# Performance work log

Hardware: AMD Instinct MI355X
Metric: run time of the kernel (lower is better)

## Reference

```python
import jax, jax.numpy as jnp
import numpy as np

N, IN_FEAT, LAT_FEAT, OUT_FEAT = 131072, 128, 128, 256
NUM_EXPERTS, TOP_K, OMEGA = 8, 2, 30.0


def setup_inputs() -> dict:
    key = jax.random.key(0)
    ks = jax.random.split(key, 8)
    u = lambda k_, shape, lim: jax.random.uniform(k_, shape, jnp.float32, -lim, lim)
    w_lim = np.sqrt(6.0 / IN_FEAT) / OMEGA  # SIREN init for non-first layers
    return {
        "x": jax.random.normal(ks[0], (N, IN_FEAT), jnp.float32),
        "latents": jax.random.normal(ks[1], (N, LAT_FEAT), jnp.float32),
        "gate_w": u(ks[2], (IN_FEAT, NUM_EXPERTS), 1.0 / np.sqrt(IN_FEAT)),
        "gate_b": jnp.zeros((NUM_EXPERTS,), jnp.float32),
        "W": u(ks[3], (NUM_EXPERTS, IN_FEAT, OUT_FEAT), w_lim),
        "b": u(ks[4], (NUM_EXPERTS, OUT_FEAT), 1.0 / np.sqrt(IN_FEAT)),
        "Wl": u(ks[5], (NUM_EXPERTS, LAT_FEAT, 2 * OUT_FEAT), 1.0 / np.sqrt(LAT_FEAT)),
        "bl": u(ks[6], (NUM_EXPERTS, 2 * OUT_FEAT), 1.0 / np.sqrt(LAT_FEAT)),
    }


def reference(x, latents, gate_w, gate_b, W, b, Wl, bl):
    # Gating: top-k over expert logits, softmax over the selected k logits.
    logits = x @ gate_w + gate_b                      # [N, E]
    top_vals, top_idx = jax.lax.top_k(logits, TOP_K)  # [N, k]
    top_w = jax.nn.softmax(top_vals, axis=-1)         # [N, k]
    # Dense combine weights: combine[n, e] = sum_i top_w[n, i] * (top_idx[n,i]==e).
    # Mathematically identical to the masked gather/scatter loop in torch.
    combine = jnp.sum(
        jax.nn.one_hot(top_idx, NUM_EXPERTS, dtype=x.dtype) * top_w[..., None],
        axis=1,
    )  # [N, E]
    out = jnp.zeros((x.shape[0], OUT_FEAT), x.dtype)
    for e in range(NUM_EXPERTS):  # fixed small loop over experts
        h = x @ W[e] + b[e]                    # [N, out]
        lat = latents @ Wl[e] + bl[e]          # [N, 2*out]
        scale, shift = lat[:, :OUT_FEAT], lat[:, OUT_FEAT:]
        out = out + combine[:, e:e + 1] * jnp.sin(OMEGA * h * scale + shift)
    return (out, latents)
```

## Files before the change

kernel.cpp:

```cpp
#include <hip/hip_runtime.h>

#define INF_  128
#define OUTF  256
#define LATF  128
#define OUT2  512
#define NEXP  8
#define OMEGA_ 30.0f

typedef float  f32x4  __attribute__((ext_vector_type(4)));
typedef __bf16 bf16x8 __attribute__((ext_vector_type(8)));
typedef unsigned short ushort8 __attribute__((ext_vector_type(8)));

#define PACK_THREADS (NEXP * 4 * 4 * 3 * 4 * 64)
#define EXP_STRIDE   (4 * 4 * 3 * 4 * 512)
#define PH_STRIDE    6144
#define GEMM_GRID    1056

__device__ __forceinline__ unsigned short bfbits(float f) {
    unsigned int u = __builtin_bit_cast(unsigned int, f);
    return (unsigned short)((u + 0x7FFFu + ((u >> 16) & 1u)) >> 16);
}

__device__ __forceinline__ bf16x8 cvt8(f32x4 a, f32x4 b) {
    bf16x8 r;
    r[0] = (__bf16)a.x; r[1] = (__bf16)a.y; r[2] = (__bf16)a.z; r[3] = (__bf16)a.w;
    r[4] = (__bf16)b.x; r[5] = (__bf16)b.y; r[6] = (__bf16)b.z; r[7] = (__bf16)b.w;
    return r;
}

#define GLOAD_LDS16(g, l) __builtin_amdgcn_global_load_lds( \
    (const __attribute__((address_space(1))) unsigned int*)(g), \
    (__attribute__((address_space(3))) unsigned int*)(l), 16, 0, 0)

__global__ void prep_kernel(const float* __restrict__ x,
                            const float* __restrict__ lat,
                            const float* __restrict__ gw,
                            const float* __restrict__ gb,
                            const float* __restrict__ W,
                            const float* __restrict__ Wl,
                            unsigned short* __restrict__ eidx,
                            float2* __restrict__ wpair,
                            unsigned int* __restrict__ cnt,
                            float* __restrict__ lat_out,
                            unsigned short* __restrict__ Bpk,
                            int nGate)
{
    __shared__ float sgw[INF_ * NEXP];
    __shared__ int lc[64];
    const int tid = threadIdx.x;

    if ((int)blockIdx.x >= nGate) {
        const int t = ((int)blockIdx.x - nGate) * 256 + tid;
        if (t >= PACK_THREADS) return;
        const int l   = t & 63;
        const int ks  = (t >> 6) & 3;
        const int m3  = (t >> 8) % 3;
        const int g   = (t >> 8) / 3;
        const int nf  = g & 3, nc = (g >> 2) & 3, e = g >> 4;
        const int col = nc * 64 + nf * 16 + (l & 15);
        const int kb  = ks * 32 + (l >> 4) * 8;
        ushort8 o;
#pragma unroll
        for (int j = 0; j < 8; ++j) {
            float v;
            if (m3 == 0) v = W [((size_t)e * 128 + kb + j) * 256 + col];
            else         v = Wl[((size_t)e * 128 + kb + j) * 512 + col + (m3 == 2 ? 256 : 0)];
            o[j] = bfbits(v);
        }
        *(ushort8*)(Bpk + (size_t)t * 8) = o;
        return;
    }

    ((float4*)sgw)[tid] = ((const float4*)gw)[tid];
    if (tid < 64) lc[tid] = 0;
    __syncthreads();

    const int t = blockIdx.x * 256 + tid;
    float acc[8];
#pragma unroll
    for (int e = 0; e < 8; ++e) acc[e] = gb[e];
    const float4* xr = (const float4*)(x + (size_t)t * INF_);
#pragma unroll 8
    for (int i = 0; i < 32; ++i) {
        float4 v = xr[i];
#pragma unroll
        for (int j = 0; j < 4; ++j) {
            const float xk = (&v.x)[j];
            const float4 g0 = *(const float4*)&sgw[(i * 4 + j) * 8];
            const float4 g1 = *(const float4*)&sgw[(i * 4 + j) * 8 + 4];
            acc[0] += xk * g0.x; acc[1] += xk * g0.y; acc[2] += xk * g0.z; acc[3] += xk * g0.w;
            acc[4] += xk * g1.x; acc[5] += xk * g1.y; acc[6] += xk * g1.z; acc[7] += xk * g1.w;
        }
    }
    float best = -1e30f, sec = -1e30f; int bi = 0, si = 0;
#pragma unroll
    for (int e = 0; e < 8; ++e) {
        const float v = acc[e];
        if (v > best)      { sec = best; si = bi; best = v; bi = e; }
        else if (v > sec)  { sec = v; si = e; }
    }
    const float ew  = __expf(sec - best);
    const float inv = 1.0f / (1.0f + ew);
    const float wb  = inv, wsc = ew * inv;
    int emin, emax; float wmin, wmax;
    if (bi < si) { emin = bi; wmin = wb;  emax = si; wmax = wsc; }
    else         { emin = si; wmin = wsc; emax = bi; wmax = wb;  }
    const int pid = emin * 8 + emax;
    eidx[t]  = (unsigned short)pid;
    wpair[t] = make_float2(wmin, wmax);
    atomicAdd(&lc[pid], 1);
    __syncthreads();
    if (tid < 64) { if (lc[tid]) atomicAdd(&cnt[tid], (unsigned int)lc[tid]); }

    const f32x4* lr = (const f32x4*)(lat) + (size_t)blockIdx.x * 8192;
    f32x4*       lo = (f32x4*)(lat_out)   + (size_t)blockIdx.x * 8192;
#pragma unroll
    for (int i = 0; i < 32; ++i) {
        f32x4 v = lr[tid + i * 256];
        __builtin_nontemporal_store(v, &lo[tid + i * 256]);
    }
}

__global__ void scan_kernel(unsigned int* __restrict__ c, unsigned int* __restrict__ table)
{
    const int p = threadIdx.x;
    const unsigned int n = c[p];
    unsigned int s = n;
#pragma unroll
    for (int d = 1; d < 64; d <<= 1) {
        unsigned int t = __shfl_up(s, d);
        if (p >= d) s += t;
    }
    const unsigned int excl = s - n;
    c[64 + p] = excl; c[128 + p] = excl;
    const unsigned int nt = (n + 127) >> 7;
    unsigned int ts = nt;
#pragma unroll
    for (int d = 1; d < 64; d <<= 1) {
        unsigned int t = __shfl_up(ts, d);
        if (p >= d) ts += t;
    }
    const unsigned int texcl = ts - nt;
    for (unsigned int t = 0; t < nt; ++t) table[texcl + t] = (unsigned int)p | (t << 6);
    if (p == 63) c[192] = texcl + nt;
}

__global__ void scatter_kernel(const unsigned short* __restrict__ eidx,
                               const float2* __restrict__ wpair,
                               unsigned int* __restrict__ cur,
                               unsigned int* __restrict__ perm,
                               float2* __restrict__ wps)
{
    __shared__ int lc[64];
    __shared__ unsigned int lbase[64];
    const int tid = threadIdx.x;
    if (tid < 64) lc[tid] = 0;
    __syncthreads();
    const int t = blockIdx.x * 256 + tid;
    const int pid = eidx[t];
    const float2 w = wpair[t];
    const int p = atomicAdd(&lc[pid], 1);
    __syncthreads();
    if (tid < 64) { lbase[tid] = lc[tid] ? atomicAdd(&cur[tid], (unsigned int)lc[tid]) : 0u; }
    __syncthreads();
    const unsigned int q = lbase[pid] + (unsigned int)p;
    perm[q] = (unsigned int)t;
    wps[q]  = w;
}

__launch_bounds__(256, 4)
__global__ void moe_gemm_kernel(const float* __restrict__ x,
                                const float* __restrict__ lat,
                                const unsigned short* __restrict__ Bpk,
                                const float* __restrict__ bias,
                                const float* __restrict__ biasl,
                                const unsigned int* __restrict__ c,
                                const unsigned int* __restrict__ table,
                                const unsigned int* __restrict__ perm,
                                const float2* __restrict__ wps,
                                float* __restrict__ out)
{
    __shared__ __align__(16) unsigned short sB[3][2 * PH_STRIDE];
    __shared__ __align__(16) float sbias[6 * 256];

    const unsigned int ntiles = c[192];
    const unsigned int d = blockIdx.x;
    const unsigned int bid = (d & 7) * (GEMM_GRID / 8) + (d >> 3);
    if (bid >= ntiles) return;
    const unsigned int ent = table[bid];
    const int pid  = ent & 63;
    const int tile = ent >> 6;
    const int emin = pid >> 3, emax = pid & 7;
    const unsigned int cn  = c[pid];
    const unsigned int off = c[64 + pid] + (unsigned int)tile * 128u;
    const int rows = min(128, (int)(cn - (unsigned int)tile * 128u));
    const unsigned int* permS = perm + off;
    const float2* wS = wps + off;

    const int tid  = threadIdx.x;
    const int lane = tid & 63;
    const int w    = tid >> 6;
    const int lrow = lane & 15;
    const int lgrp = lane >> 4;
    const int half = tid >> 7;
    const int wh   = (tid >> 6) & 1;
    const int t7   = tid & 127;

    const int r0 = w * 32 + lrow, r1 = r0 + 16;
    const int t0 = (int)permS[min(r0, rows - 1)];
    const int t1 = (int)permS[min(r1, rows - 1)];
    const float2 w0 = wS[min(r0, rows - 1)];
    const float2 w1 = wS[min(r1, rows - 1)];
    bf16x8 ax[2][4], al[2][4];
    {
        const float* x0 = x   + (size_t)t0 * INF_;
        const float* x1 = x   + (size_t)t1 * INF_;
        const float* l0 = lat + (size_t)t0 * LATF;
        const float* l1 = lat + (size_t)t1 * LATF;
#pragma unroll
        for (int ks = 0; ks < 4; ++ks) {
            const int kb = ks * 32 + lgrp * 8;
            ax[0][ks] = cvt8(__builtin_nontemporal_load((const f32x4*)(x0 + kb)),
                             __builtin_nontemporal_load((const f32x4*)(x0 + kb + 4)));
            ax[1][ks] = cvt8(__builtin_nontemporal_load((const f32x4*)(x1 + kb)),
                             __builtin_nontemporal_load((const f32x4*)(x1 + kb + 4)));
            al[0][ks] = cvt8(__builtin_nontemporal_load((const f32x4*)(l0 + kb)),
                             __builtin_nontemporal_load((const f32x4*)(l0 + kb + 4)));
            al[1][ks] = cvt8(__builtin_nontemporal_load((const f32x4*)(l1 + kb)),
                             __builtin_nontemporal_load((const f32x4*)(l1 + kb + 4)));
        }
    }

    const unsigned short* B0 = Bpk + (size_t)emin * EXP_STRIDE;
    const unsigned short* B1 = Bpk + (size_t)emax * EXP_STRIDE;
    const unsigned short* Bh = half ? B1 : B0;

    {
        const float* bsrc =
            (w == 0) ? bias  + emin * OUTF :
            (w == 1) ? bias  + emax * OUTF :
            (w == 2) ? biasl + emin * OUT2 :
                       biasl + emin * OUT2 + 256;
        GLOAD_LDS16(bsrc + lane * 4, &sbias[w * 256]);
        if (w < 2) {
            const float* bsrc2 = (w == 0) ? biasl + emax * OUT2
                                          : biasl + emax * OUT2 + 256;
            GLOAD_LDS16(bsrc2 + lane * 4, &sbias[(4 + w) * 256]);
        }
    }

    auto STAGE = [&](int ph, int buf) {
        const unsigned short* src = Bh + (size_t)ph * PH_STRIDE + (size_t)t7 * 8;
        unsigned short* dst = &sB[buf][half * PH_STRIDE + wh * 512];
#pragma unroll
        for (int r = 0; r < 6; ++r)
            GLOAD_LDS16(src + r * 1024, dst + r * 1024);
    };

    f32x4 acc[2][3][2];
    auto COMPUTE = [&](int ph, int buf) {
        const int cb = ph * 16 + lgrp * 4;
        const f32x4 b0h = *(const f32x4*)&sbias[0 * 256 + cb];
        const f32x4 b1h = *(const f32x4*)&sbias[1 * 256 + cb];
        const f32x4 b0s = *(const f32x4*)&sbias[2 * 256 + cb];
        const f32x4 b0f = *(const f32x4*)&sbias[3 * 256 + cb];
        const f32x4 b1s = *(const f32x4*)&sbias[4 * 256 + cb];
        const f32x4 b1f = *(const f32x4*)&sbias[5 * 256 + cb];
#pragma unroll
        for (int mf = 0; mf < 2; ++mf) {
            acc[0][0][mf] = b0h; acc[0][1][mf] = b0s; acc[0][2][mf] = b0f;
            acc[1][0][mf] = b1h; acc[1][1][mf] = b1s; acc[1][2][mf] = b1f;
        }
#pragma unroll
        for (int ex = 0; ex < 2; ++ex) {
#pragma unroll
            for (int m = 0; m < 3; ++m) {
                bf16x8 bb[4];
#pragma unroll
                for (int ks = 0; ks < 4; ++ks)
                    bb[ks] = *(const bf16x8*)&sB[buf][ex * PH_STRIDE + (m * 4 + ks) * 512 + lane * 8];
#pragma unroll
                for (int ks = 0; ks < 4; ++ks) {
#pragma unroll
                    for (int mf = 0; mf < 2; ++mf) {
                        const bf16x8 a = (m == 0) ? ax[mf][ks] : al[mf][ks];
                        acc[ex][m][mf] = __builtin_amdgcn_mfma_f32_16x16x32_bf16(bb[ks], a, acc[ex][m][mf], 0, 0, 0);
                    }
                }
            }
        }
    };

    auto EPILOGUE = [&](int ph, bool guard) {
        const int cb = ph * 16 + lgrp * 4;
#pragma unroll
        for (int mf = 0; mf < 2; ++mf) {
            const int  rr  = mf ? r1 : r0;
            if (guard && rr >= rows) continue;
            const int  tok = mf ? t1 : t0;
            const float wmn = mf ? w1.x : w0.x;
            const float wmx = mf ? w1.y : w0.y;
            const f32x4 h0 = acc[0][0][mf], s0 = acc[0][1][mf], f0 = acc[0][2][mf];
            const f32x4 h1 = acc[1][0][mf], s1 = acc[1][1][mf], f1 = acc[1][2][mf];
            f32x4 v;
#pragma unroll
            for (int j = 0; j < 4; ++j) {
                v[j] = wmn * __sinf(OMEGA_ * h0[j] * s0[j] + f0[j])
                     + wmx * __sinf(OMEGA_ * h1[j] * s1[j] + f1[j]);
            }
            __builtin_nontemporal_store(v, (f32x4*)(out + (size_t)tok * OUTF + cb));
        }
    };

    if (rows == 128) {
        STAGE(0, 0);
        STAGE(1, 1);
        asm volatile("s_waitcnt vmcnt(6)" ::: "memory");
        __builtin_amdgcn_s_barrier();
        __builtin_amdgcn_sched_barrier(0);
#pragma unroll 1
        for (int ph = 0; ph < 16; ++ph) {
            const int buf = ph % 3;
            if (ph < 14) STAGE(ph + 2, (ph + 2) % 3);
            COMPUTE(ph, buf);
            EPILOGUE(ph, false);
            __builtin_amdgcn_sched_barrier(0);
            if (ph == 0)       asm volatile("s_waitcnt vmcnt(8)" ::: "memory");
            else if (ph < 14)  asm volatile("s_waitcnt vmcnt(10)" ::: "memory");
            else if (ph == 14) asm volatile("s_waitcnt vmcnt(4)" ::: "memory");
            if (ph < 15) {
                __builtin_amdgcn_s_barrier();
                __builtin_amdgcn_sched_barrier(0);
            }
        }
    } else {
#pragma unroll 1
        for (int ph = 0; ph < 16; ++ph) {
            const int buf = ph % 3;
            STAGE(ph, buf);
            asm volatile("s_waitcnt vmcnt(0)" ::: "memory");
            __builtin_amdgcn_s_barrier();
            __builtin_amdgcn_sched_barrier(0);
            COMPUTE(ph, buf);
            EPILOGUE(ph, true);
            __builtin_amdgcn_s_barrier();
            __builtin_amdgcn_sched_barrier(0);
        }
    }
}

extern "C" void kernel_launch(void* const* d_in, const int* in_sizes, int n_in,
                              void* d_out, int out_size, void* d_ws, size_t ws_size,
                              hipStream_t stream)
{
    const float* x   = (const float*)d_in[0];
    const float* lat = (const float*)d_in[1];
    const float* gw  = (const float*)d_in[2];
    const float* gb  = (const float*)d_in[3];
    const float* W   = (const float*)d_in[4];
    const float* b   = (const float*)d_in[5];
    const float* Wl  = (const float*)d_in[6];
    const float* bl  = (const float*)d_in[7];
    float* out = (float*)d_out;
    const int N = in_sizes[0] / INF_;

    char* ws = (char*)d_ws;
    unsigned int*   cnt   = (unsigned int*)ws;
    unsigned int*   table = (unsigned int*)(ws + 1024);
    unsigned short* eidx  = (unsigned short*)(ws + 8192);
    float2*         wpair = (float2*)(ws + 8192 + 2 * (size_t)N);
    unsigned int*   perm  = (unsigned int*)(ws + 8192 + 10 * (size_t)N);
    float2*         wps   = (float2*)(ws + 8192 + 14 * (size_t)N);
    unsigned short* Bpk   = (unsigned short*)(ws + 8192 + 22 * (size_t)N);

    (void)hipMemsetAsync(cnt, 0, 256, stream);

    const int nGate = N / 256;
    prep_kernel<<<dim3(nGate + PACK_THREADS / 256), 256, 0, stream>>>(
        x, lat, gw, gb, W, Wl, eidx, wpair, cnt, out + (size_t)N * OUTF, Bpk, nGate);
    scan_kernel<<<1, 64, 0, stream>>>(cnt, table);
    scatter_kernel<<<dim3(N / 256), 256, 0, stream>>>(eidx, wpair, cnt + 128, perm, wps);

    moe_gemm_kernel<<<dim3(GEMM_GRID), 256, 0, stream>>>(x, lat, Bpk, b, bl,
                                                         cnt, table, perm, wps, out);
}
```

Baseline: 162.6 us.

## Switch B staging to double buffering, store bias as bf16, add bias in epilogue

Moves the B-weight LDS pipeline from triple to double buffering with a one-phase prefetch, cutting LDS use. Bias is converted to bf16 in shared memory and added in the epilogue instead of seeding the accumulators. Launch bounds drop to 3 waves per SIMD. This frees registers and LDS but shortens the prefetch depth and adds bf16 rounding to the bias.

```diff
diff --git a/kernel.cpp b/kernel.cpp
--- a/kernel.cpp
+++ b/kernel.cpp
@@ -25,6 +25,16 @@
     bf16x8 r;
     r[0] = (__bf16)a.x; r[1] = (__bf16)a.y; r[2] = (__bf16)a.z; r[3] = (__bf16)a.w;
     r[4] = (__bf16)b.x; r[5] = (__bf16)b.y; r[6] = (__bf16)b.z; r[7] = (__bf16)b.w;
+    return r;
+}
+
+__device__ __forceinline__ f32x4 bload(const unsigned short* p) {
+    const ushort4 u = *(const ushort4*)p;
+    f32x4 r;
+    r.x = __builtin_bit_cast(float, (unsigned int)u.x << 16);
+    r.y = __builtin_bit_cast(float, (unsigned int)u.y << 16);
+    r.z = __builtin_bit_cast(float, (unsigned int)u.z << 16);
+    r.w = __builtin_bit_cast(float, (unsigned int)u.w << 16);
     return r;
 }
 
@@ -168,7 +178,7 @@
     wps[q]  = w;
 }
 
-__launch_bounds__(256, 4)
+__launch_bounds__(256, 3)
 __global__ void moe_gemm_kernel(const float* __restrict__ x,
                                 const float* __restrict__ lat,
                                 const unsigned short* __restrict__ Bpk,
@@ -180,8 +190,8 @@
                                 const float2* __restrict__ wps,
                                 float* __restrict__ out)
 {
-    __shared__ __align__(16) unsigned short sB[3][2 * PH_STRIDE];
-    __shared__ __align__(16) float sbias[6 * 256];
+    __shared__ __align__(16) unsigned short sB[2][2 * PH_STRIDE];
+    __shared__ __align__(16) unsigned short sbias[6 * 256];
 
     const unsigned int ntiles = c[192];
     const unsigned int d = blockIdx.x;
@@ -236,16 +246,24 @@
     const unsigned short* Bh = half ? B1 : B0;
 
     {
-        const float* bsrc =
-            (w == 0) ? bias  + emin * OUTF :
-            (w == 1) ? bias  + emax * OUTF :
-            (w == 2) ? biasl + emin * OUT2 :
-                       biasl + emin * OUT2 + 256;
-        GLOAD_LDS16(bsrc + lane * 4, &sbias[w * 256]);
-        if (w < 2) {
-            const float* bsrc2 = (w == 0) ? biasl + emax * OUT2
-                                          : biasl + emax * OUT2 + 256;
-            GLOAD_LDS16(bsrc2 + lane * 4, &sbias[(4 + w) * 256]);
+        const int i4 = (tid & 63) * 4;
+        const int sg = tid >> 6;
+#pragma unroll
+        for (int rep = 0; rep < 2; ++rep) {
+            const int seg = sg + rep * 4;
+            if (seg < 6) {
+                const float* bsrc =
+                    (seg == 0) ? bias  + emin * OUTF :
+                    (seg == 1) ? bias  + emax * OUTF :
+                    (seg == 2) ? biasl + emin * OUT2 :
+                    (seg == 3) ? biasl + emin * OUT2 + 256 :
+                    (seg == 4) ? biasl + emax * OUT2 :
+                                 biasl + emax * OUT2 + 256;
+                const f32x4 v = *(const f32x4*)(bsrc + i4);
+                ushort4 u;
+                u.x = bfbits(v.x); u.y = bfbits(v.y); u.z = bfbits(v.z); u.w = bfbits(v.w);
+                *(ushort4*)&sbias[seg * 256 + i4] = u;
+            }
         }
     }
 
@@ -258,19 +276,13 @@
     };
 
     f32x4 acc[2][3][2];
-    auto COMPUTE = [&](int ph, int buf) {
-        const int cb = ph * 16 + lgrp * 4;
-        const f32x4 b0h = *(const f32x4*)&sbias[0 * 256 + cb];
-        const f32x4 b1h = *(const f32x4*)&sbias[1 * 256 + cb];
-        const f32x4 b0s = *(const f32x4*)&sbias[2 * 256 + cb];
-        const f32x4 b0f = *(const f32x4*)&sbias[3 * 256 + cb];
-        const f32x4 b1s = *(const f32x4*)&sbias[4 * 256 + cb];
-        const f32x4 b1f = *(const f32x4*)&sbias[5 * 256 + cb];
-#pragma unroll
-        for (int mf = 0; mf < 2; ++mf) {
-            acc[0][0][mf] = b0h; acc[0][1][mf] = b0s; acc[0][2][mf] = b0f;
-            acc[1][0][mf] = b1h; acc[1][1][mf] = b1s; acc[1][2][mf] = b1f;
-        }
+    auto COMPUTE = [&](int buf) {
+#pragma unroll
+        for (int ex = 0; ex < 2; ++ex)
+#pragma unroll
+            for (int m = 0; m < 3; ++m)
+#pragma unroll
+                for (int mf = 0; mf < 2; ++mf) acc[ex][m][mf] = (f32x4)0.0f;
 #pragma unroll
         for (int ex = 0; ex < 2; ++ex) {
 #pragma unroll
@@ -293,6 +305,12 @@
 
     auto EPILOGUE = [&](int ph, bool guard) {
         const int cb = ph * 16 + lgrp * 4;
+        const f32x4 b0h = bload(&sbias[0 * 256 + cb]);
+        const f32x4 b1h = bload(&sbias[1 * 256 + cb]);
+        const f32x4 b0s = bload(&sbias[2 * 256 + cb]);
+        const f32x4 b0f = bload(&sbias[3 * 256 + cb]);
+        const f32x4 b1s = bload(&sbias[4 * 256 + cb]);
+        const f32x4 b1f = bload(&sbias[5 * 256 + cb]);
 #pragma unroll
         for (int mf = 0; mf < 2; ++mf) {
             const int  rr  = mf ? r1 : r0;
@@ -300,35 +318,37 @@
             const int  tok = mf ? t1 : t0;
             const float wmn = mf ? w1.x : w0.x;
             const float wmx = mf ? w1.y : w0.y;
-            const f32x4 h0 = acc[0][0][mf], s0 = acc[0][1][mf], f0 = acc[0][2][mf];
-            const f32x4 h1 = acc[1][0][mf], s1 = acc[1][1][mf], f1 = acc[1][2][mf];
             f32x4 v;
 #pragma unroll
             for (int j = 0; j < 4; ++j) {
-                v[j] = wmn * __sinf(OMEGA_ * h0[j] * s0[j] + f0[j])
-                     + wmx * __sinf(OMEGA_ * h1[j] * s1[j] + f1[j]);
+                const float h0 = acc[0][0][mf][j] + b0h[j];
+                const float s0 = acc[0][1][mf][j] + b0s[j];
+                const float f0 = acc[0][2][mf][j] + b0f[j];
+                const float h1 = acc[1][0][mf][j] + b1h[j];
+                const float s1 = acc[1][1][mf][j] + b1s[j];
+                const float f1 = acc[1][2][mf][j] + b1f[j];
+                v[j] = wmn * __sinf(OMEGA_ * h0 * s0 + f0)
+                     + wmx * __sinf(OMEGA_ * h1 * s1 + f1);
             }
             __builtin_nontemporal_store(v, (f32x4*)(out + (size_t)tok * OUTF + cb));
         }
     };
 
+    STAGE(0, 0);
+    asm volatile("s_waitcnt vmcnt(0) lgkmcnt(0)" ::: "memory");
+    __builtin_amdgcn_s_barrier();
+    __builtin_amdgcn_sched_barrier(0);
+
     if (rows == 128) {
-        STAGE(0, 0);
-        STAGE(1, 1);
-        asm volatile("s_waitcnt vmcnt(6)" ::: "memory");
-        __builtin_amdgcn_s_barrier();
-        __builtin_amdgcn_sched_barrier(0);
 #pragma unroll 1
         for (int ph = 0; ph < 16; ++ph) {
-            const int buf = ph % 3;
-            if (ph < 14) STAGE(ph + 2, (ph + 2) % 3);
-            COMPUTE(ph, buf);
+            const int buf = ph & 1;
+            if (ph < 15) STAGE(ph + 1, buf ^ 1);
+            COMPUTE(buf);
             EPILOGUE(ph, false);
             __builtin_amdgcn_sched_barrier(0);
-            if (ph == 0)       asm volatile("s_waitcnt vmcnt(8)" ::: "memory");
-            else if (ph < 14)  asm volatile("s_waitcnt vmcnt(10)" ::: "memory");
-            else if (ph == 14) asm volatile("s_waitcnt vmcnt(4)" ::: "memory");
             if (ph < 15) {
+                asm volatile("s_waitcnt vmcnt(2)" ::: "memory");
                 __builtin_amdgcn_s_barrier();
                 __builtin_amdgcn_sched_barrier(0);
             }
@@ -336,12 +356,14 @@
     } else {
 #pragma unroll 1
         for (int ph = 0; ph < 16; ++ph) {
-            const int buf = ph % 3;
-            STAGE(ph, buf);
-            asm volatile("s_waitcnt vmcnt(0)" ::: "memory");
-            __builtin_amdgcn_s_barrier();
-            __builtin_amdgcn_sched_barrier(0);
-            COMPUTE(ph, buf);
+            const int buf = ph & 1;
+            if (ph > 0) {
+                STAGE(ph, buf);
+                asm volatile("s_waitcnt vmcnt(0)" ::: "memory");
+                __builtin_amdgcn_s_barrier();
+                __builtin_amdgcn_sched_barrier(0);
+            }
+            COMPUTE(buf);
             EPILOGUE(ph, true);
             __builtin_amdgcn_s_barrier();
             __builtin_amdgcn_sched_barrier(0);
```

Result: no change. 164.0 us (+0.9%).
